# Kernel optimization log

Hardware: AMD Instinct MI355X
Metric: run time of the kernel (lower is better)

## Reference

```python
import jax, jax.numpy as jnp
import numpy as np

N_NODES = 10000
N_EDGES = 640000
F_IN = 128
HID = 128
F_OUT = 40
BN_EPS = 1e-5


def setup_inputs() -> dict:
    key = jax.random.key(0)
    ks = jax.random.split(key, 8)
    x = jax.random.normal(ks[0], (N_NODES, F_IN), dtype=jnp.float32)
    edge_row = jax.random.randint(ks[1], (N_EDGES,), 0, N_NODES)
    edge_col = jax.random.randint(ks[2], (N_EDGES,), 0, N_NODES)
    edge_val = jax.random.uniform(ks[3], (N_EDGES,), dtype=jnp.float32)
    W1 = jax.random.normal(ks[4], (F_IN, HID), dtype=jnp.float32) * 0.05
    W2 = jax.random.normal(ks[5], (HID, HID), dtype=jnp.float32) * 0.05
    W3 = jax.random.normal(ks[6], (HID, F_OUT), dtype=jnp.float32) * 0.05
    return {
        "x": x, "edge_row": edge_row, "edge_col": edge_col, "edge_val": edge_val,
        "W1": W1, "b1": jnp.zeros((HID,), jnp.float32),
        "gamma2": jnp.ones((HID,), jnp.float32), "beta2": jnp.zeros((HID,), jnp.float32),
        "W2": W2, "b2": jnp.zeros((HID,), jnp.float32),
        "gamma3": jnp.ones((HID,), jnp.float32), "beta3": jnp.zeros((HID,), jnp.float32),
        "W3": W3, "b3": jnp.zeros((F_OUT,), jnp.float32),
    }


def _spmm(edge_row, edge_col, edge_val, x, n_nodes):
    # out[i] = sum_{e: row[e]==i} val[e] * x[col[e]]  == torch.sparse.mm(adj, x)
    msgs = edge_val[:, None] * jnp.take(x, edge_col, axis=0)  # [E, F]
    return jax.ops.segment_sum(msgs, edge_row, num_segments=n_nodes)


def _batchnorm(x, gamma, beta):
    # BatchNorm1d (training-mode normalization, biased variance)
    mean = jnp.mean(x, axis=0)
    var = jnp.mean(jnp.square(x - mean), axis=0)
    return gamma * (x - mean) * jax.lax.rsqrt(var + BN_EPS) + beta


def reference(x, edge_row, edge_col, edge_val, W1, b1, gamma2, beta2,
              W2, b2, gamma3, beta3, W3, b3):
    n = x.shape[0]
    # layer 1: SpMM -> Linear -> ReLU -> (dropout=identity in eval) -> BN
    h = _spmm(edge_row, edge_col, edge_val, x, n)
    h = jax.nn.relu(h @ W1 + b1)
    h = _batchnorm(h, gamma2, beta2)
    # layer 2
    h = _spmm(edge_row, edge_col, edge_val, h, n)
    h = jax.nn.relu(h @ W2 + b2)
    h = _batchnorm(h, gamma3, beta3)
    # layer 3
    h = _spmm(edge_row, edge_col, edge_val, h, n)
    h = h @ W3 + b3
    return jax.nn.log_softmax(h, axis=1)
```

## Files before the change

### kernel.cpp

```cpp
#include <hip/hip_runtime.h>
#include <hip/hip_bf16.h>
#include <math.h>

#define N_NODES 10000
#define F 128
#define F_OUT_ 40
#define N_EDGES_ 640000
#define BN_EPS 1e-5f
#define NBIN 625
#define RPB 16
#define NWGA 64
#define EPW 10000
#define BINCAP 1536

__device__ __forceinline__ unsigned pack4(int col, float v) {
    __hip_bfloat16 b = __float2bfloat16(v);
    return ((unsigned)(*(unsigned short*)&b) << 16) | (unsigned)col;
}
__device__ __forceinline__ int   col_of(unsigned q) { return (int)(q & 0xFFFFu); }
__device__ __forceinline__ float val_of(unsigned q) { return __uint_as_float(q & 0xFFFF0000u); }

__global__ __launch_bounds__(256) void fused_g1h(const float* __restrict__ x,
        const float* __restrict__ W1, __hip_bfloat16* __restrict__ T,
        const int* __restrict__ erow, int* __restrict__ hist) {
    __shared__ float Ws[F * F];
    __shared__ float As[16][F];
    __shared__ int   lh[NBIN];
    int tid = threadIdx.x;
    if (blockIdx.x >= NBIN) {
        int w = blockIdx.x - NBIN;
        for (int t = tid; t < NBIN; t += 256) lh[t] = 0;
        __syncthreads();
        int e0 = w * EPW;
        for (int e = e0 + tid; e < e0 + EPW; e += 256)
            atomicAdd(&lh[erow[e] >> 4], 1);
        __syncthreads();
        for (int t = tid; t < NBIN; t += 256) hist[w * NBIN + t] = lh[t];
        return;
    }
    for (int i = tid; i < F * F; i += 256) Ws[i] = W1[i];
    int r0 = blockIdx.x * 16;
    for (int i = tid; i < 16 * F; i += 256) {
        int r2 = i >> 7, k = i & (F - 1);
        As[r2][k] = x[(size_t)(r0 + r2) * F + k];
    }
    __syncthreads();
    int c = tid & (F - 1), hh = tid >> 7;
    for (int r2 = hh; r2 < 16; r2 += 2) {
        float acc = 0.f;
        #pragma unroll
        for (int k = 0; k < F; ++k) acc = fmaf(As[r2][k], Ws[k * F + c], acc);
        T[(size_t)(r0 + r2) * F + c] = __float2bfloat16(acc);
    }
}

__global__ __launch_bounds__(64) void scan_w(const int* __restrict__ hist,
                                             int* __restrict__ offs,
                                             int* __restrict__ totals) {
    int b = blockIdx.x, t = threadIdx.x;
    int h = hist[t * NBIN + b];
    int v = h;
    #pragma unroll
    for (int off = 1; off < 64; off <<= 1) {
        int u = __shfl_up(v, off);
        if (t >= off) v += u;
    }
    offs[t * NBIN + b] = v - h;
    if (t == 63) totals[b] = v;
}

__global__ __launch_bounds__(1024) void scan_bins(const int* __restrict__ totals,
                                                  int* __restrict__ base) {
    __shared__ int sc[1024];
    int tid = threadIdx.x;
    int val = (tid < NBIN) ? totals[tid] : 0;
    sc[tid] = val;
    __syncthreads();
    for (int off = 1; off < 1024; off <<= 1) {
        int v = 0;
        if (tid >= off) v = sc[tid - off];
        __syncthreads();
        if (tid >= off) sc[tid] += v;
        __syncthreads();
    }
    if (tid < NBIN) base[tid] = sc[tid] - val;
    if (tid == NBIN - 1) base[NBIN] = sc[tid];
}

__global__ __launch_bounds__(256) void scatter_bin(const int* __restrict__ erow,
                                                   const int* __restrict__ ecol,
                                                   const float* __restrict__ eval_,
                                                   const int* __restrict__ offs,
                                                   const int* __restrict__ base,
                                                   int2* __restrict__ ebin) {
    __shared__ int myoff[NBIN];
    __shared__ int cur[NBIN];
    int w = blockIdx.x, tid = threadIdx.x;
    for (int t = tid; t < NBIN; t += 256) {
        myoff[t] = base[t] + offs[w * NBIN + t];
        cur[t] = 0;
    }
    __syncthreads();
    int e0 = w * EPW;
    for (int e = e0 + tid; e < e0 + EPW; e += 256) {
        int r = erow[e];
        int b = r >> 4;
        int p = atomicAdd(&cur[b], 1);
        ebin[myoff[b] + p] = make_int2((r << 14) | ecol[e], __float_as_int(eval_[e]));
    }
}

__global__ __launch_bounds__(256) void sort_bin(const int* __restrict__ base,
                                                const int2* __restrict__ ebin,
                                                unsigned* __restrict__ ebin2,
                                                int* __restrict__ rowptr) {
    __shared__ int2    ein[BINCAP];
    __shared__ unsigned eout[BINCAP];
    __shared__ int cnt16[16], pos16[16], exc[16];
    int b = blockIdx.x, tid = threadIdx.x;
    int lo = base[b], hi = base[b + 1];
    int n = min(hi - lo, BINCAP);
    for (int i = tid; i < n; i += 256) ein[i] = ebin[lo + i];
    if (tid < 16) cnt16[tid] = 0;
    __syncthreads();
    for (int i = tid; i < n; i += 256)
        atomicAdd(&cnt16[(ein[i].x >> 14) & 15], 1);
    __syncthreads();
    if (tid == 0) {
        int run = 0;
        #pragma unroll
        for (int j = 0; j < 16; ++j) { exc[j] = run; run += cnt16[j]; }
    }
    __syncthreads();
    if (tid < 16) {
        pos16[tid] = exc[tid];
        rowptr[b * RPB + tid] = lo + exc[tid];
    }
    if (b == NBIN - 1 && tid == 0) rowptr[N_NODES] = hi;
    __syncthreads();
    for (int i = tid; i < n; i += 256) {
        int2 q = ein[i];
        int j = (q.x >> 14) & 15;
        int p = atomicAdd(&pos16[j], 1);
        eout[p] = pack4(q.x & 16383, __int_as_float(q.y));
    }
    __syncthreads();
    for (int i = tid; i < n; i += 256) ebin2[lo + i] = eout[i];
}

__global__ __launch_bounds__(256) void spmm_row2(const int* __restrict__ rowptr,
                                                 const unsigned* __restrict__ epk,
                                                 const unsigned int* __restrict__ T,
                                                 float* __restrict__ Z,
                                                 float* __restrict__ accs) {
    if (blockIdx.x == 0 && threadIdx.x < 256) accs[threadIdx.x] = 0.f;
    __shared__ float2 sbuf[4][64];
    int wv   = threadIdx.x >> 6;
    int lane = threadIdx.x & 63;
    int r    = blockIdx.x * 2 + (wv >> 1);
    int half = wv & 1;
    bool valid = (r < N_NODES);
    float ev = 0.f, od = 0.f;
    if (valid) {
        int beg = rowptr[r], end = rowptr[r + 1];
        int mid = (beg + end) >> 1;
        int b = half ? mid : beg;
        int e = half ? end : mid;
        const unsigned int* Tb = T + lane;
        float se[4] = {0.f, 0.f, 0.f, 0.f};
        float so[4] = {0.f, 0.f, 0.f, 0.f};
        int i = b;
        int n8 = b + ((e - b) & ~7);
        for (; i < n8; i += 8) {
            unsigned q[8]; unsigned int w[8];
            #pragma unroll
            for (int j = 0; j < 8; ++j) q[j] = epk[i + j];
            #pragma unroll
            for (int j = 0; j < 8; ++j) w[j] = Tb[(unsigned)col_of(q[j]) * 64u];
            #pragma unroll
            for (int j = 0; j < 8; ++j) {
                float v = val_of(q[j]);
                se[j & 3] = fmaf(v, __uint_as_float(w[j] << 16), se[j & 3]);
                so[j & 3] = fmaf(v, __uint_as_float(w[j] & 0xffff0000u), so[j & 3]);
            }
        }
        for (; i < e; ++i) {
            unsigned q = epk[i];
            unsigned int w = Tb[(unsigned)col_of(q) * 64u];
            float v = val_of(q);
            se[0] = fmaf(v, __uint_as_float(w << 16), se[0]);
            so[0] = fmaf(v, __uint_as_float(w & 0xffff0000u), so[0]);
        }
        ev = (se[0] + se[1]) + (se[2] + se[3]);
        od = (so[0] + so[1]) + (so[2] + so[3]);
    }
    sbuf[wv][lane] = make_float2(ev, od);
    __syncthreads();
    if ((wv & 1) == 0 && valid) {
        float2 a = sbuf[wv][lane], b2 = sbuf[wv + 1][lane];
        *(float2*)(Z + (size_t)r * F + 2 * lane) = make_float2(a.x + b2.x, a.y + b2.y);
    }
}

__global__ __launch_bounds__(256) void spmm40_ls(const int* __restrict__ rowptr,
                                                 const unsigned* __restrict__ epk,
                                                 const unsigned short* __restrict__ T40,
                                                 const float* __restrict__ b3,
                                                 float* __restrict__ out) {
    int w = blockIdx.x * 4 + (threadIdx.x >> 6);
    int lane = threadIdx.x & 63;
    if (w >= N_NODES) return;
    float acc = 0.f;
    if (lane < F_OUT_) {
        const unsigned short* Tb = T40 + lane;
        int beg = rowptr[w], end = rowptr[w + 1];
        float a[4] = {0.f, 0.f, 0.f, 0.f};
        int i = beg;
        int n4 = beg + ((end - beg) & ~3);
        for (; i < n4; i += 4) {
            unsigned q[4]; unsigned short u[4];
            #pragma unroll
            for (int j = 0; j < 4; ++j) q[j] = epk[i + j];
            #pragma unroll
            for (int j = 0; j < 4; ++j) u[j] = Tb[(unsigned)col_of(q[j]) * 40u];
            #pragma unroll
            for (int j = 0; j < 4; ++j)
                a[j] = fmaf(val_of(q[j]), __uint_as_float(((unsigned)u[j]) << 16), a[j]);
        }
        for (; i < end; ++i) {
            unsigned q = epk[i];
            unsigned short u = Tb[(unsigned)col_of(q) * 40u];
            a[0] = fmaf(val_of(q), __uint_as_float(((unsigned)u) << 16), a[0]);
        }
        acc = (a[0] + a[1]) + (a[2] + a[3]) + b3[lane];
    }
    float val = (lane < F_OUT_) ? acc : -INFINITY;
    float m = val;
    #pragma unroll
    for (int off = 32; off > 0; off >>= 1) m = fmaxf(m, __shfl_xor(m, off));
    float e = (lane < F_OUT_) ? expf(val - m) : 0.f;
    float s = e;
    #pragma unroll
    for (int off = 32; off > 0; off >>= 1) s += __shfl_xor(s, off);
    if (lane < F_OUT_) out[(size_t)w * F_OUT_ + lane] = val - m - logf(s);
}


__global__ void bn_stats_br(const float* __restrict__ X, const float* __restrict__ bias,
                            float* __restrict__ acc) {
    int f = threadIdx.x & (F - 1);
    float b = bias[f];
    float s = 0.f, s2 = 0.f;
    long long total = (long long)N_NODES * F;
    long long stride = (long long)gridDim.x * blockDim.x;
    for (long long idx = (long long)blockIdx.x * blockDim.x + threadIdx.x;
         idx < total; idx += stride) {
        float t = fmaxf(X[idx] + b, 0.f);
        s += t; s2 += t * t;
    }
    __shared__ float ls[256], ls2[256];
    ls[threadIdx.x] = s; ls2[threadIdx.x] = s2;
    __syncthreads();
    if (threadIdx.x < 128) {
        s  = ls[threadIdx.x] + ls[threadIdx.x + 128];
        s2 = ls2[threadIdx.x] + ls2[threadIdx.x + 128];
        atomicAdd(&acc[f], s);
        atomicAdd(&acc[F + f], s2);
    }
}


__global__ __launch_bounds__(256) void gemm128_bn(const float* __restrict__ A,
        const float* __restrict__ W, const float* __restrict__ bias,
        const float* __restrict__ gamma, const float* __restrict__ beta,
        const float* __restrict__ accs, __hip_bfloat16* __restrict__ C) {
    __shared__ float Ws[F * F];
    __shared__ float As[16][F];
    __shared__ float sc[F], sh[F], bi[F];
    int tid = threadIdx.x;
    if (tid < F) {
        float m   = accs[tid] / (float)N_NODES;
        float var = accs[F + tid] / (float)N_NODES - m * m;
        float rs  = rsqrtf(var + BN_EPS);
        float g   = gamma[tid] * rs;
        sc[tid] = g;
        sh[tid] = beta[tid] - g * m;
        bi[tid] = bias[tid];
    }
    for (int i = tid; i < F * F; i += 256) Ws[i] = W[i];
    __syncthreads();
    int r0 = blockIdx.x * 16;
    for (int i = tid; i < 16 * F; i += 256) {
        int r2 = i >> 7, k = i & (F - 1);
        float a = A[(size_t)(r0 + r2) * F + k];
        As[r2][k] = fmaxf(a + bi[k], 0.f) * sc[k] + sh[k];
    }
    __syncthreads();
    int c = tid & (F - 1), hh = tid >> 7;
    for (int r2 = hh; r2 < 16; r2 += 2) {
        float acc = 0.f;
        #pragma unroll
        for (int k = 0; k < F; ++k) acc = fmaf(As[r2][k], Ws[k * F + c], acc);
        C[(size_t)(r0 + r2) * F + c] = __float2bfloat16(acc);
    }
}

__global__ __launch_bounds__(256) void gemm40_bn(const float* __restrict__ A,
        const float* __restrict__ W, const float* __restrict__ bias,
        const float* __restrict__ gamma, const float* __restrict__ beta,
        const float* __restrict__ accs, __hip_bfloat16* __restrict__ C) {
    __shared__ float Ws[F * F_OUT_];
    __shared__ float sc[F], sh[F], bi[F];
    int tid = threadIdx.x;
    if (tid < F) {
        float m   = accs[tid] / (float)N_NODES;
        float var = accs[F + tid] / (float)N_NODES - m * m;
        float rs  = rsqrtf(var + BN_EPS);
        float g   = gamma[tid] * rs;
        sc[tid] = g;
        sh[tid] = beta[tid] - g * m;
        bi[tid] = bias[tid];
    }
    for (int i = tid; i < F * F_OUT_; i += 256) Ws[i] = W[i];
    __syncthreads();
    int c = tid % F_OUT_, rl = tid / F_OUT_;
    if (rl >= 6) return;
    int r = blockIdx.x * 6 + rl;
    if (r >= N_NODES) return;
    const float* a = A + (size_t)r * F;
    float acc = 0.f;
    #pragma unroll
    for (int k = 0; k < F; ++k) {
        float t = fmaxf(a[k] + bi[k], 0.f) * sc[k] + sh[k];
        acc = fmaf(t, Ws[k * F_OUT_ + c], acc);
    }
    C[(size_t)r * F_OUT_ + c] = __float2bfloat16(acc);
}


extern "C" void kernel_launch(void* const* d_in, const int* in_sizes, int n_in,
                              void* d_out, int out_size, void* d_ws, size_t ws_size,
                              hipStream_t stream) {
    const float* x      = (const float*)d_in[0];
    const int*   erow   = (const int*)  d_in[1];
    const int*   ecol   = (const int*)  d_in[2];
    const float* eval_  = (const float*)d_in[3];
    const float* W1     = (const float*)d_in[4];
    const float* b1     = (const float*)d_in[5];
    const float* gamma2 = (const float*)d_in[6];
    const float* beta2  = (const float*)d_in[7];
    const float* W2     = (const float*)d_in[8];
    const float* b2     = (const float*)d_in[9];
    const float* gamma3 = (const float*)d_in[10];
    const float* beta3  = (const float*)d_in[11];
    const float* W3     = (const float*)d_in[12];
    const float* b3     = (const float*)d_in[13];
    float* out = (float*)d_out;

    const size_t nf = (size_t)N_NODES * F;
    const int BLK = 256;

    int*   hist   = (int*)d_ws;
    int*   offs   = hist + NWGA * NBIN;
    int*   totals = offs + NWGA * NBIN;
    int*   base   = totals + 640;
    float* accs   = (float*)(base + 640);
    int*   rowptr = (int*)(accs + 256);
    __hip_bfloat16* T = (__hip_bfloat16*)(rowptr + 10016);
    float* Z     = (float*)((char*)T + nf * 2);
    int2*  ebin  = (int2*)(Z + nf);
    unsigned* ebin2 = (unsigned*)(ebin + N_EDGES_);

    fused_g1h<<<NBIN + NWGA, BLK, 0, stream>>>(x, W1, T, erow, hist);
    scan_w<<<NBIN, 64, 0, stream>>>(hist, offs, totals);
    scan_bins<<<1, 1024, 0, stream>>>(totals, base);
    scatter_bin<<<NWGA, BLK, 0, stream>>>(erow, ecol, eval_, offs, base, ebin);
    sort_bin<<<NBIN, BLK, 0, stream>>>(base, ebin, ebin2, rowptr);

    const int GB2  = (N_NODES + 1) / 2;
    const int GB40 = (N_NODES + 3) / 4;

    spmm_row2<<<GB2, BLK, 0, stream>>>(rowptr, ebin2, (const unsigned int*)T, Z, accs);
    bn_stats_br<<<256, BLK, 0, stream>>>(Z, b1, accs);

    gemm128_bn<<<NBIN, BLK, 0, stream>>>(Z, W2, b1, gamma2, beta2, accs, T);
    spmm_row2<<<GB2, BLK, 0, stream>>>(rowptr, ebin2, (const unsigned int*)T, Z, accs);
    bn_stats_br<<<256, BLK, 0, stream>>>(Z, b2, accs);

    gemm40_bn<<<(N_NODES + 5) / 6, BLK, 0, stream>>>(Z, W3, b2, gamma3, beta3, accs, T);
    spmm40_ls<<<GB40, BLK, 0, stream>>>(rowptr, ebin2, (const unsigned short*)T, b3, out);
}
```

Before: 173.0 us.

## Load edge chunks cooperatively and broadcast via shuffles, one wave per row

The SpMM kernels now have each wavefront load up to 64 packed edges with one coalesced load and broadcast each edge to all lanes with __shfl, instead of every lane loading the same edge words. The 128-wide SpMM also drops the two-wave-per-row split and its shared-memory reduction, assigning one full row per wave with 16-way unrolled gathers. This cuts redundant edge loads and a block barrier but removes the intra-row parallelism that halved each wave's work, and adds register pressure from the larger unroll.

Result: faster. 165.5 us (-4.3%).

```diff
diff --git a/kernel.cpp b/kernel.cpp
--- a/kernel.cpp
+++ b/kernel.cpp
@@ -19,6 +19,8 @@
 }
 __device__ __forceinline__ int   col_of(unsigned q) { return (int)(q & 0xFFFFu); }
 __device__ __forceinline__ float val_of(unsigned q) { return __uint_as_float(q & 0xFFFF0000u); }
+__device__ __forceinline__ float lo16f(unsigned w) { return __uint_as_float(w << 16); }
+__device__ __forceinline__ float hi16f(unsigned w) { return __uint_as_float(w & 0xffff0000u); }
 
 __global__ __launch_bounds__(256) void fused_g1h(const float* __restrict__ x,
         const float* __restrict__ W1, __hip_bfloat16* __restrict__ T,
@@ -148,58 +150,49 @@
     for (int i = tid; i < n; i += 256) ebin2[lo + i] = eout[i];
 }
 
-__global__ __launch_bounds__(256) void spmm_row2(const int* __restrict__ rowptr,
+__global__ __launch_bounds__(256) void spmm_row3(const int* __restrict__ rowptr,
                                                  const unsigned* __restrict__ epk,
-                                                 const unsigned int* __restrict__ T,
+                                                 const unsigned* __restrict__ T,
                                                  float* __restrict__ Z,
                                                  float* __restrict__ accs) {
     if (blockIdx.x == 0 && threadIdx.x < 256) accs[threadIdx.x] = 0.f;
-    __shared__ float2 sbuf[4][64];
-    int wv   = threadIdx.x >> 6;
-    int lane = threadIdx.x & 63;
-    int r    = blockIdx.x * 2 + (wv >> 1);
-    int half = wv & 1;
-    bool valid = (r < N_NODES);
-    float ev = 0.f, od = 0.f;
-    if (valid) {
-        int beg = rowptr[r], end = rowptr[r + 1];
-        int mid = (beg + end) >> 1;
-        int b = half ? mid : beg;
-        int e = half ? end : mid;
-        const unsigned int* Tb = T + lane;
-        float se[4] = {0.f, 0.f, 0.f, 0.f};
-        float so[4] = {0.f, 0.f, 0.f, 0.f};
-        int i = b;
-        int n8 = b + ((e - b) & ~7);
-        for (; i < n8; i += 8) {
-            unsigned q[8]; unsigned int w[8];
+    int wv = threadIdx.x >> 6, lane = threadIdx.x & 63;
+    int r = blockIdx.x * 4 + wv;
+    if (r >= N_NODES) return;
+    int beg = rowptr[r], end = rowptr[r + 1];
+    const unsigned* Tb = T + lane;
+    float se[4] = {0.f, 0.f, 0.f, 0.f};
+    float so[4] = {0.f, 0.f, 0.f, 0.f};
+    for (int base = beg; base < end; base += 64) {
+        int m = min(end - base, 64);
+        unsigned myq = 0;
+        if (lane < m) myq = epk[base + lane];
+        int j = 0;
+        for (; j + 16 <= m; j += 16) {
+            unsigned w[16]; float v[16];
             #pragma unroll
-            for (int j = 0; j < 8; ++j) q[j] = epk[i + j];
+            for (int t = 0; t < 16; ++t) {
+                unsigned q = __shfl(myq, j + t);
+                v[t] = val_of(q);
+                w[t] = Tb[(unsigned)col_of(q) * 64u];
+            }
             #pragma unroll
-            for (int j = 0; j < 8; ++j) w[j] = Tb[(unsigned)col_of(q[j]) * 64u];
-            #pragma unroll
-            for (int j = 0; j < 8; ++j) {
-                float v = val_of(q[j]);
-                se[j & 3] = fmaf(v, __uint_as_float(w[j] << 16), se[j & 3]);
-                so[j & 3] = fmaf(v, __uint_as_float(w[j] & 0xffff0000u), so[j & 3]);
+            for (int t = 0; t < 16; ++t) {
+                se[t & 3] = fmaf(v[t], lo16f(w[t]), se[t & 3]);
+                so[t & 3] = fmaf(v[t], hi16f(w[t]), so[t & 3]);
             }
         }
-        for (; i < e; ++i) {
-            unsigned q = epk[i];
-            unsigned int w = Tb[(unsigned)col_of(q) * 64u];
+        for (; j < m; ++j) {
+            unsigned q = __shfl(myq, j);
+            unsigned w = Tb[(unsigned)col_of(q) * 64u];
             float v = val_of(q);
-            se[0] = fmaf(v, __uint_as_float(w << 16), se[0]);
-            so[0] = fmaf(v, __uint_as_float(w & 0xffff0000u), so[0]);
+            se[0] = fmaf(v, lo16f(w), se[0]);
+            so[0] = fmaf(v, hi16f(w), so[0]);
         }
-        ev = (se[0] + se[1]) + (se[2] + se[3]);
-        od = (so[0] + so[1]) + (so[2] + so[3]);
-    }
-    sbuf[wv][lane] = make_float2(ev, od);
-    __syncthreads();
-    if ((wv & 1) == 0 && valid) {
-        float2 a = sbuf[wv][lane], b2 = sbuf[wv + 1][lane];
-        *(float2*)(Z + (size_t)r * F + 2 * lane) = make_float2(a.x + b2.x, a.y + b2.y);
-    }
+    }
+    float ev = (se[0] + se[1]) + (se[2] + se[3]);
+    float od = (so[0] + so[1]) + (so[2] + so[3]);
+    *(float2*)(Z + (size_t)r * F + 2 * lane) = make_float2(ev, od);
 }
 
 __global__ __launch_bounds__(256) void spmm40_ls(const int* __restrict__ rowptr,
@@ -207,42 +200,50 @@
                                                  const unsigned short* __restrict__ T40,
                                                  const float* __restrict__ b3,
                                                  float* __restrict__ out) {
-    int w = blockIdx.x * 4 + (threadIdx.x >> 6);
-    int lane = threadIdx.x & 63;
+    int wv = threadIdx.x >> 6, lane = threadIdx.x & 63;
+    int w = blockIdx.x * 4 + wv;
     if (w >= N_NODES) return;
-    float acc = 0.f;
-    if (lane < F_OUT_) {
-        const unsigned short* Tb = T40 + lane;
-        int beg = rowptr[w], end = rowptr[w + 1];
-        float a[4] = {0.f, 0.f, 0.f, 0.f};
-        int i = beg;
-        int n4 = beg + ((end - beg) & ~3);
-        for (; i < n4; i += 4) {
-            unsigned q[4]; unsigned short u[4];
+    int beg = rowptr[w], end = rowptr[w + 1];
+    float a[4] = {0.f, 0.f, 0.f, 0.f};
+    const unsigned short* Tb = T40 + lane;
+    bool act = (lane < F_OUT_);
+    for (int base = beg; base < end; base += 64) {
+        int m = min(end - base, 64);
+        unsigned myq = 0;
+        if (lane < m) myq = epk[base + lane];
+        int j = 0;
+        for (; j + 8 <= m; j += 8) {
+            unsigned q[8];
             #pragma unroll
-            for (int j = 0; j < 4; ++j) q[j] = epk[i + j];
-            #pragma unroll
-            for (int j = 0; j < 4; ++j) u[j] = Tb[(unsigned)col_of(q[j]) * 40u];
-            #pragma unroll
-            for (int j = 0; j < 4; ++j)
-                a[j] = fmaf(val_of(q[j]), __uint_as_float(((unsigned)u[j]) << 16), a[j]);
+            for (int t = 0; t < 8; ++t) q[t] = __shfl(myq, j + t);
+            if (act) {
+                unsigned short u[8];
+                #pragma unroll
+                for (int t = 0; t < 8; ++t) u[t] = Tb[(unsigned)col_of(q[t]) * 40u];
+                #pragma unroll
+                for (int t = 0; t < 8; ++t)
+                    a[t & 3] = fmaf(val_of(q[t]),
+                                    __uint_as_float(((unsigned)u[t]) << 16), a[t & 3]);
+            }
         }
-        for (; i < end; ++i) {
-            unsigned q = epk[i];
-            unsigned short u = Tb[(unsigned)col_of(q) * 40u];
-            a[0] = fmaf(val_of(q), __uint_as_float(((unsigned)u) << 16), a[0]);
+        for (; j < m; ++j) {
+            unsigned q = __shfl(myq, j);
+            if (act) {
+                unsigned short u = Tb[(unsigned)col_of(q) * 40u];
+                a[0] = fmaf(val_of(q), __uint_as_float(((unsigned)u) << 16), a[0]);
+            }
         }
-        acc = (a[0] + a[1]) + (a[2] + a[3]) + b3[lane];
-    }
-    float val = (lane < F_OUT_) ? acc : -INFINITY;
-    float m = val;
+    }
+    float acc = (a[0] + a[1]) + (a[2] + a[3]);
+    float val = act ? acc + b3[lane] : -INFINITY;
+    float m2 = val;
     #pragma unroll
-    for (int off = 32; off > 0; off >>= 1) m = fmaxf(m, __shfl_xor(m, off));
-    float e = (lane < F_OUT_) ? expf(val - m) : 0.f;
+    for (int off = 32; off > 0; off >>= 1) m2 = fmaxf(m2, __shfl_xor(m2, off));
+    float e = act ? expf(val - m2) : 0.f;
     float s = e;
     #pragma unroll
     for (int off = 32; off > 0; off >>= 1) s += __shfl_xor(s, off);
-    if (lane < F_OUT_) out[(size_t)w * F_OUT_ + lane] = val - m - logf(s);
+    if (act) out[(size_t)w * F_OUT_ + lane] = val - m2 - logf(s);
 }
 
 
@@ -377,16 +378,15 @@
     scatter_bin<<<NWGA, BLK, 0, stream>>>(erow, ecol, eval_, offs, base, ebin);
     sort_bin<<<NBIN, BLK, 0, stream>>>(base, ebin, ebin2, rowptr);
 
-    const int GB2  = (N_NODES + 1) / 2;
-    const int GB40 = (N_NODES + 3) / 4;
-
-    spmm_row2<<<GB2, BLK, 0, stream>>>(rowptr, ebin2, (const unsigned int*)T, Z, accs);
+    const int GB4 = (N_NODES + 3) / 4;
+
+    spmm_row3<<<GB4, BLK, 0, stream>>>(rowptr, ebin2, (const unsigned*)T, Z, accs);
     bn_stats_br<<<256, BLK, 0, stream>>>(Z, b1, accs);
 
     gemm128_bn<<<NBIN, BLK, 0, stream>>>(Z, W2, b1, gamma2, beta2, accs, T);
-    spmm_row2<<<GB2, BLK, 0, stream>>>(rowptr, ebin2, (const unsigned int*)T, Z, accs);
+    spmm_row3<<<GB4, BLK, 0, stream>>>(rowptr, ebin2, (const unsigned*)T, Z, accs);
     bn_stats_br<<<256, BLK, 0, stream>>>(Z, b2, accs);
 
     gemm40_bn<<<(N_NODES + 5) / 6, BLK, 0, stream>>>(Z, W3, b2, gamma3, beta3, accs, T);
-    spmm40_ls<<<GB40, BLK, 0, stream>>>(rowptr, ebin2, (const unsigned short*)T, b3, out);
-}
+    spmm40_ls<<<GB4, BLK, 0, stream>>>(rowptr, ebin2, (const unsigned short*)T, b3, out);
+}
```
